# Optimization experiments

Hardware: AMD Instinct MI355X
Metric: run time of the kernel (lower is better)

Reference implementation:

```python
import jax, jax.numpy as jnp
import numpy as np
from jax import lax

N = 100000      # nodes
F_IN = 128      # dataset.num_features
H = 64          # hidden
E = 1600000     # edges
G = 1000        # graphs (equal-sized, contiguous)
PER = N // G    # nodes per graph = 100
K = 30          # sort-pool k
KS = 3          # conv1d kernel = num_layers


def setup_inputs() -> dict:
    key = jax.random.key(0)
    ks = jax.random.split(key, 20)
    lin = lambda k, i, o: (jax.random.normal(k, (i, o), jnp.float32) / np.sqrt(i)).astype(jnp.float32)
    return {
        "x": jax.random.normal(ks[0], (N, F_IN), jnp.float32),
        "src": jax.random.randint(ks[1], (E,), 0, N, dtype=jnp.int32),
        "dst": jax.random.randint(ks[2], (E,), 0, N, dtype=jnp.int32),
        "num_graphs": G,
        # SAGEConv 1: lin_l (aggr, with bias), lin_r (self, no bias)
        "wl1": lin(ks[3], F_IN, H), "wr1": lin(ks[4], F_IN, H), "b1": jnp.zeros((H,), jnp.float32),
        "wl2": lin(ks[5], H, H), "wr2": lin(ks[6], H, H), "b2": jnp.zeros((H,), jnp.float32),
        "wl3": lin(ks[7], H, H), "wr3": lin(ks[8], H, H), "b3": jnp.zeros((H,), jnp.float32),
        # Conv1d(hidden=64 -> 32, kernel=3): weight [O, I, K]
        "cw": (jax.random.normal(ks[9], (32, H, KS), jnp.float32) / np.sqrt(H * KS)).astype(jnp.float32),
        "cb": jnp.zeros((32,), jnp.float32),
        "w1": lin(ks[10], 32 * (K - KS + 1), H), "bb1": jnp.zeros((H,), jnp.float32),
        "w2": lin(ks[11], H, 1), "bb2": jnp.zeros((1,), jnp.float32),
    }


def _sage(x, src, dst, wl, wr, b, n):
    # PyG SAGEConv (mean aggr): lin_l(mean_{j->i} x_j) + lin_r(x_i)
    msum = jax.ops.segment_sum(x[src], dst, num_segments=n)           # [N, F]
    cnt = jax.ops.segment_sum(jnp.ones((src.shape[0],), x.dtype), dst, num_segments=n)
    mean = msum / jnp.maximum(cnt, 1.0)[:, None]
    return mean @ wl + b + x @ wr


def reference(x, src, dst, num_graphs, wl1, wr1, b1, wl2, wr2, b2, wl3, wr3, b3, cw, cb, w1, bb1, w2, bb2):
    n = x.shape[0]
    h = jax.nn.relu(_sage(x, src, dst, wl1, wr1, b1, n))
    h = jax.nn.relu(_sage(h, src, dst, wl2, wr2, b2, n))
    h = jax.nn.relu(_sage(h, src, dst, wl3, wr3, b3, n))
    # SortAggregation(k): per-graph, sort nodes by last feature channel (desc), keep top-k.
    # batch = contiguous equal-sized graphs -> dense reshape is exact.
    hg = h.reshape(num_graphs, PER, H)                                # [G, PER, H]
    order = jnp.argsort(-hg[:, :, -1], axis=1)[:, :K]                 # [G, K]
    topk = jnp.take_along_axis(hg, order[:, :, None], axis=1)         # [G, K, H]
    xc = jnp.transpose(topk, (0, 2, 1))                               # [G, H, K]
    y = lax.conv_general_dilated(xc, cw, (1,), 'VALID',
                                 dimension_numbers=('NCH', 'OIH', 'NCH'))
    y = jax.nn.relu(y + cb[None, :, None])                            # [G, 32, K-KS+1]
    y = y.reshape(num_graphs, -1)
    y = jax.nn.relu(y @ w1 + bb1)
    # dropout: eval mode -> identity
    return y @ w2 + bb2                                               # [G, 1]
```

## Files before the change

kernel.cpp:

```cpp
#include <hip/hip_runtime.h>

#define NN 100000
#define EE 1600000
#define GG 1000
#define PERG 100
#define KK 30
#define HH 64

#define NB 782
#define CAP 4096
#define CHB 4096

__global__ __launch_bounds__(1024) void zero_int(int* p, int n) {
  int i = blockIdx.x * 1024 + threadIdx.x;
  if (i < n) p[i] = 0;
}

__global__ __launch_bounds__(256) void bucket_kernel(const int* __restrict__ src,
                                                     const int* __restrict__ dst,
                                                     int* __restrict__ gcur,
                                                     int* __restrict__ pairs) {
  __shared__ int lhist[NB];
  __shared__ int lbase[NB];
  __shared__ int lcur[NB];
  const int t = threadIdx.x;
  const int c0 = blockIdx.x * CHB;
  const int c1 = min(c0 + CHB, EE);
  for (int b = t; b < NB; b += 256) {
    lhist[b] = 0;
    lcur[b] = 0;
  }
  __syncthreads();
  for (int e = c0 + t; e < c1; e += 256) atomicAdd(&lhist[dst[e] >> 7], 1);
  __syncthreads();
  for (int b = t; b < NB; b += 256) {
    int c = lhist[b];
    lbase[b] = c ? atomicAdd(&gcur[b], c) : 0;
  }
  __syncthreads();
  for (int e = c0 + t; e < c1; e += 256) {
    int d = dst[e];
    int b = d >> 7;
    int p = atomicAdd(&lcur[b], 1);
    pairs[b * CAP + lbase[b] + p] = (src[e] << 7) | (d & 127);
  }
}

__global__ __launch_bounds__(1024) void bucket_scan(const int* __restrict__ gcur,
                                                    int* __restrict__ bbase) {
  __shared__ int tmp[1024];
  const int t = threadIdx.x;
  int v = (t < NB) ? gcur[t] : 0;
  tmp[t] = v;
  __syncthreads();
  for (int off = 1; off < 1024; off <<= 1) {
    int u = (t >= off) ? tmp[t - off] : 0;
    __syncthreads();
    tmp[t] += u;
    __syncthreads();
  }
  if (t < NB) bbase[t] = tmp[t] - v;
}

__global__ __launch_bounds__(256) void csr_kernel(const int* __restrict__ gcur,
                                                  const int* __restrict__ bbase,
                                                  const int* __restrict__ pairs,
                                                  int* __restrict__ row_start,
                                                  int* __restrict__ cnt,
                                                  int* __restrict__ eidx) {
  __shared__ int vals[CAP];
  __shared__ int hist[128];
  __shared__ int offs[128];
  __shared__ int cur[128];
  const int b = blockIdx.x;
  const int t = threadIdx.x;
  const int nb = gcur[b];
  const int base = bbase[b];
  if (t < 128) {
    hist[t] = 0;
    cur[t] = 0;
  }
  __syncthreads();
  for (int i = t; i < nb; i += 256) {
    int v = pairs[b * CAP + i];
    vals[i] = v;
    atomicAdd(&hist[v & 127], 1);
  }
  __syncthreads();
  if (t < 128) {
    int s = 0;
    for (int m = 0; m < t; ++m) s += hist[m];
    offs[t] = s;
    int node = b * 128 + t;
    if (node < NN) {
      row_start[node] = base + s;
      cnt[node] = hist[t];
    }
  }
  __syncthreads();
  for (int i = t; i < nb; i += 256) {
    int v = vals[i];
    int ld = v & 127;
    int p = atomicAdd(&cur[ld], 1);
    eidx[base + offs[ld] + p] = v >> 7;
  }
}

template <int K>
__global__ __launch_bounds__(256) void proj_kernel(const float* __restrict__ X,
                                                   const float* __restrict__ WL,
                                                   const float* __restrict__ WR,
                                                   float* __restrict__ P,
                                                   float* __restrict__ R) {
  constexpr int BM = 128, BK = 32, XSP = 40, WSP = 144;
  __shared__ float xs[BM * XSP];
  __shared__ float ws[BK * WSP];
  const int t = threadIdx.x;
  const int row0 = blockIdx.x * BM;
  const int tc = t & 15, tr = t >> 4;
  const int wcol = tc * 8 + (tc >> 2) * 4;

  float acc[8][8];
#pragma unroll
  for (int i = 0; i < 8; ++i)
#pragma unroll
    for (int j = 0; j < 8; ++j) acc[i][j] = 0.f;

  for (int k0 = 0; k0 < K; k0 += BK) {
    __syncthreads();
    for (int idx = t; idx < BM * 8; idx += 256) {
      int r = idx >> 3, c = idx & 7;
      int row = row0 + r;
      float4 v = make_float4(0.f, 0.f, 0.f, 0.f);
      if (row < NN) v = *reinterpret_cast<const float4*>(&X[(size_t)row * K + k0 + c * 4]);
      *reinterpret_cast<float4*>(&xs[r * XSP + c * 4]) = v;
    }
    for (int idx = t; idx < BK * 16; idx += 256) {
      int kr = idx >> 4, c4 = idx & 15;
      int gcl = c4 >> 1;
      int off = gcl * 8 + (gcl >> 2) * 4 + (c4 & 1) * 4;
      *reinterpret_cast<float4*>(&ws[kr * WSP + off]) =
          *reinterpret_cast<const float4*>(&WL[(k0 + kr) * 64 + c4 * 4]);
      int g2 = gcl + 8;
      int off2 = g2 * 8 + (g2 >> 2) * 4 + (c4 & 1) * 4;
      *reinterpret_cast<float4*>(&ws[kr * WSP + off2]) =
          *reinterpret_cast<const float4*>(&WR[(k0 + kr) * 64 + c4 * 4]);
    }
    __syncthreads();
    for (int kk4 = 0; kk4 < BK; kk4 += 4) {
      float4 a[8];
#pragma unroll
      for (int i = 0; i < 8; ++i)
        a[i] = *reinterpret_cast<const float4*>(&xs[(tr + 16 * i) * XSP + kk4]);
#pragma unroll
      for (int kk = 0; kk < 4; ++kk) {
        float4 b0 = *reinterpret_cast<const float4*>(&ws[(kk4 + kk) * WSP + wcol]);
        float4 b1 = *reinterpret_cast<const float4*>(&ws[(kk4 + kk) * WSP + wcol + 4]);
        float bv[8] = {b0.x, b0.y, b0.z, b0.w, b1.x, b1.y, b1.z, b1.w};
#pragma unroll
        for (int i = 0; i < 8; ++i) {
          float av = (kk == 0) ? a[i].x : (kk == 1) ? a[i].y : (kk == 2) ? a[i].z : a[i].w;
#pragma unroll
          for (int j = 0; j < 8; ++j) acc[i][j] = fmaf(av, bv[j], acc[i][j]);
        }
      }
    }
  }

  float* OUT = (tc < 8) ? P : R;
  int cb = (tc & 7) * 8;
#pragma unroll
  for (int i = 0; i < 8; ++i) {
    int row = row0 + tr + 16 * i;
    if (row < NN) {
      *reinterpret_cast<float4*>(&OUT[(size_t)row * 64 + cb]) =
          make_float4(acc[i][0], acc[i][1], acc[i][2], acc[i][3]);
      *reinterpret_cast<float4*>(&OUT[(size_t)row * 64 + cb + 4]) =
          make_float4(acc[i][4], acc[i][5], acc[i][6], acc[i][7]);
    }
  }
}

__global__ __launch_bounds__(256) void agg_kernel(const float* __restrict__ P,
                                                  const float* __restrict__ R,
                                                  const float* __restrict__ bias,
                                                  const int* __restrict__ row_start,
                                                  const int* __restrict__ cnt,
                                                  const int* __restrict__ eidx,
                                                  float* __restrict__ h,
                                                  float* __restrict__ keys) {
  int wid = (blockIdx.x * 256 + threadIdx.x) >> 6;
  int lane = threadIdx.x & 63;
  if (wid >= NN) return;
  const int q = lane >> 4;
  const int ql = lane & 15;
  const int base = row_start[wid];
  const int deg = cnt[wid];
  float4 a0 = make_float4(0.f, 0.f, 0.f, 0.f);
  float4 a1 = make_float4(0.f, 0.f, 0.f, 0.f);

  for (int e0 = 0; e0 < deg; e0 += 64) {
    const int m = min(64, deg - e0);
    int idx = (lane < m) ? eidx[base + e0 + lane] : 0;
    for (int j = 0; j < m; j += 16) {
      const int eA = j + q, eB = j + 4 + q, eC = j + 8 + q, eD = j + 12 + q;
      const int sA = __shfl(idx, min(eA, m - 1));
      const int sB = __shfl(idx, min(eB, m - 1));
      const int sC = __shfl(idx, min(eC, m - 1));
      const int sD = __shfl(idx, min(eD, m - 1));
      const float wA = (eA < m) ? 1.f : 0.f;
      const float wB = (eB < m) ? 1.f : 0.f;
      const float wC = (eC < m) ? 1.f : 0.f;
      const float wD = (eD < m) ? 1.f : 0.f;
      float4 vA = *reinterpret_cast<const float4*>(&P[(size_t)sA * 64 + ql * 4]);
      float4 vB = *reinterpret_cast<const float4*>(&P[(size_t)sB * 64 + ql * 4]);
      float4 vC = *reinterpret_cast<const float4*>(&P[(size_t)sC * 64 + ql * 4]);
      float4 vD = *reinterpret_cast<const float4*>(&P[(size_t)sD * 64 + ql * 4]);
      a0.x = fmaf(wA, vA.x, a0.x); a0.y = fmaf(wA, vA.y, a0.y);
      a0.z = fmaf(wA, vA.z, a0.z); a0.w = fmaf(wA, vA.w, a0.w);
      a1.x = fmaf(wB, vB.x, a1.x); a1.y = fmaf(wB, vB.y, a1.y);
      a1.z = fmaf(wB, vB.z, a1.z); a1.w = fmaf(wB, vB.w, a1.w);
      a0.x = fmaf(wC, vC.x, a0.x); a0.y = fmaf(wC, vC.y, a0.y);
      a0.z = fmaf(wC, vC.z, a0.z); a0.w = fmaf(wC, vC.w, a0.w);
      a1.x = fmaf(wD, vD.x, a1.x); a1.y = fmaf(wD, vD.y, a1.y);
      a1.z = fmaf(wD, vD.z, a1.z); a1.w = fmaf(wD, vD.w, a1.w);
    }
  }

  float4 acc = make_float4(a0.x + a1.x, a0.y + a1.y, a0.z + a1.z, a0.w + a1.w);
#pragma unroll
  for (int d = 16; d < 64; d <<= 1) {
    acc.x += __shfl_xor(acc.x, d);
    acc.y += __shfl_xor(acc.y, d);
    acc.z += __shfl_xor(acc.z, d);
    acc.w += __shfl_xor(acc.w, d);
  }

  if (q == 0) {
    const float dv = fmaxf((float)deg, 1.0f);
    float4 r4 = *reinterpret_cast<const float4*>(&R[(size_t)wid * 64 + ql * 4]);
    float4 b4 = *reinterpret_cast<const float4*>(&bias[ql * 4]);
    float4 o;
    o.x = fmaxf(acc.x / dv + b4.x + r4.x, 0.f);
    o.y = fmaxf(acc.y / dv + b4.y + r4.y, 0.f);
    o.z = fmaxf(acc.z / dv + b4.z + r4.z, 0.f);
    o.w = fmaxf(acc.w / dv + b4.w + r4.w, 0.f);
    *reinterpret_cast<float4*>(&h[(size_t)wid * 64 + ql * 4]) = o;
    if (keys != nullptr && ql == 15) keys[wid] = o.w;
  }
}

__global__ __launch_bounds__(256) void head_kernel(const float* __restrict__ h,
                                                   const float* __restrict__ keysArr,
                                                   const float* __restrict__ cw,
                                                   const float* __restrict__ cb,
                                                   const float* __restrict__ w1,
                                                   const float* __restrict__ bb1,
                                                   const float* __restrict__ w2,
                                                   const float* __restrict__ bb2,
                                                   float* __restrict__ out) {
  __shared__ float key[PERG];
  __shared__ int sel[KK];
  __shared__ float feat[34 * 65];
  __shared__ float cwT[192 * 33];
  __shared__ float z[896];
  __shared__ float psum[256];
  const int g = blockIdx.x;
  const int t = threadIdx.x;

  for (int idx = t; idx < 32 * 192; idx += 256) {
    int o = idx / 192, k = idx % 192;
    cwT[k * 33 + o] = cw[idx];
  }
  if (t < PERG) key[t] = keysArr[g * PERG + t];
  __syncthreads();

  if (t < PERG) {
    float kv = key[t];
    int r = 0;
    for (int m = 0; m < PERG; ++m) {
      float km = key[m];
      r += (int)((km > kv) || (km == kv && m < t));
    }
    if (r < KK) sel[r] = t;
  }
  __syncthreads();

  for (int idx = t; idx < KK * HH; idx += 256) {
    int r = idx >> 6, f = idx & 63;
    feat[r * 65 + f] = h[(size_t)(g * PERG + sel[r]) * HH + f];
  }
  __syncthreads();

  {
    const int o = t & 31;
    const int pg = t >> 5;
    float zacc[4] = {0.f, 0.f, 0.f, 0.f};
    int i = 0, tt = 0;
    for (int k = 0; k < 192; ++k) {
      float c = cwT[k * 33 + o];
#pragma unroll
      for (int j = 0; j < 4; ++j) {
        int p = pg + 8 * j;
        zacc[j] = fmaf(c, feat[(p + tt) * 65 + i], zacc[j]);
      }
      if (++tt == 3) {
        tt = 0;
        ++i;
      }
    }
    float cbo = cb[o];
#pragma unroll
    for (int j = 0; j < 4; ++j) {
      int p = pg + 8 * j;
      if (p < 28) z[o * 28 + p] = fmaxf(zacc[j] + cbo, 0.f);
    }
  }
  __syncthreads();

  {
    const int hh = t & 63;
    const int quarter = t >> 6;
    const int q0 = quarter * 224;
    float acc = 0.f;
    for (int q = 0; q < 224; ++q)
      acc = fmaf(z[q0 + q], w1[(size_t)(q0 + q) * 64 + hh], acc);
    psum[t] = acc;
  }
  __syncthreads();

  if (t < 64) {
    float o1 = fmaxf(bb1[t] + psum[t] + psum[t + 64] + psum[t + 128] + psum[t + 192], 0.f);
    float v = o1 * w2[t];
#pragma unroll
    for (int off = 32; off > 0; off >>= 1) v += __shfl_down(v, off);
    if (t == 0) out[g] = v + bb2[0];
  }
}

extern "C" void kernel_launch(void* const* d_in, const int* in_sizes, int n_in,
                              void* d_out, int out_size, void* d_ws, size_t ws_size,
                              hipStream_t stream) {
  const float* x = (const float*)d_in[0];
  const int* src = (const int*)d_in[1];
  const int* dst = (const int*)d_in[2];
  const float* wl1 = (const float*)d_in[4];
  const float* wr1 = (const float*)d_in[5];
  const float* b1 = (const float*)d_in[6];
  const float* wl2 = (const float*)d_in[7];
  const float* wr2 = (const float*)d_in[8];
  const float* b2 = (const float*)d_in[9];
  const float* wl3 = (const float*)d_in[10];
  const float* wr3 = (const float*)d_in[11];
  const float* b3 = (const float*)d_in[12];
  const float* cw = (const float*)d_in[13];
  const float* cb = (const float*)d_in[14];
  const float* w1 = (const float*)d_in[15];
  const float* bb1 = (const float*)d_in[16];
  const float* w2 = (const float*)d_in[17];
  const float* bb2 = (const float*)d_in[18];
  float* out = (float*)d_out;

  char* w = (char*)d_ws;
  auto carve = [&](size_t bytes) {
    char* p = w;
    w += (bytes + 255) & ~(size_t)255;
    return p;
  };
  int* row_start = (int*)carve((size_t)NN * 4);
  int* cnt = (int*)carve((size_t)NN * 4);
  int* eidx = (int*)carve((size_t)EE * 4);
  float* P = (float*)carve((size_t)NN * 64 * 4);
  float* R = (float*)carve((size_t)NN * 64 * 4);
  float* hbuf = (float*)carve((size_t)NN * 64 * 4);
  float* keys = (float*)carve((size_t)NN * 4);
  int* gcur = (int*)carve((size_t)NB * 4);
  int* bbase = (int*)carve((size_t)NB * 4);
  int* pairs = (int*)P;

  zero_int<<<1, 1024, 0, stream>>>(gcur, NB);
  bucket_kernel<<<(EE + CHB - 1) / CHB, 256, 0, stream>>>(src, dst, gcur, pairs);
  bucket_scan<<<1, 1024, 0, stream>>>(gcur, bbase);
  csr_kernel<<<NB, 256, 0, stream>>>(gcur, bbase, pairs, row_start, cnt, eidx);

  const int projGrid = (NN + 127) / 128;
  const int aggGrid = (NN + 3) / 4;
  proj_kernel<128><<<projGrid, 256, 0, stream>>>(x, wl1, wr1, P, R);
  agg_kernel<<<aggGrid, 256, 0, stream>>>(P, R, b1, row_start, cnt, eidx, hbuf, nullptr);
  proj_kernel<64><<<projGrid, 256, 0, stream>>>(hbuf, wl2, wr2, P, R);
  agg_kernel<<<aggGrid, 256, 0, stream>>>(P, R, b2, row_start, cnt, eidx, hbuf, nullptr);
  proj_kernel<64><<<projGrid, 256, 0, stream>>>(hbuf, wl3, wr3, P, R);
  agg_kernel<<<aggGrid, 256, 0, stream>>>(P, R, b3, row_start, cnt, eidx, hbuf, keys);
  head_kernel<<<GG, 256, 0, stream>>>(hbuf, keys, cw, cb, w1, bb1, w2, bb2, out);
}
```

Baseline: 491.1 us.

## Fuse edge bucketing with first projection and fold bucket scan into CSR

The edge bucketing pass and the first-layer projection GEMM now run as one launch, with blocks split by index so the two independent jobs share the GPU. The bucket-offset scan kernel is removed: each CSR block computes its own base by reducing the preceding bucket counts. The pairs scratch moves from P to hbuf so it does not collide with the projection outputs. This saves two launches and lets the scatter and GEMM overlap, at the cost of redundant prefix reads in every CSR block and a larger shared allocation for the bucket blocks.

```diff
diff --git a/kernel.cpp b/kernel.cpp
--- a/kernel.cpp
+++ b/kernel.cpp
@@ -10,21 +10,24 @@
 #define NB 782
 #define CAP 4096
 #define CHB 4096
+#define BUCKET_BLOCKS ((EE + CHB - 1) / CHB)
+#define PROJ_BLOCKS ((NN + 127) / 128)
 
 __global__ __launch_bounds__(1024) void zero_int(int* p, int n) {
   int i = blockIdx.x * 1024 + threadIdx.x;
   if (i < n) p[i] = 0;
 }
 
-__global__ __launch_bounds__(256) void bucket_kernel(const int* __restrict__ src,
-                                                     const int* __restrict__ dst,
-                                                     int* __restrict__ gcur,
-                                                     int* __restrict__ pairs) {
-  __shared__ int lhist[NB];
-  __shared__ int lbase[NB];
-  __shared__ int lcur[NB];
+__device__ __forceinline__ void bucket_body(int bid, float* smem,
+                                            const int* __restrict__ src,
+                                            const int* __restrict__ dst,
+                                            int* __restrict__ gcur,
+                                            int* __restrict__ pairs) {
+  int* lhist = (int*)smem;
+  int* lbase = lhist + NB;
+  int* lcur = lbase + NB;
   const int t = threadIdx.x;
-  const int c0 = blockIdx.x * CHB;
+  const int c0 = bid * CHB;
   const int c1 = min(c0 + CHB, EE);
   for (int b = t; b < NB; b += 256) {
     lhist[b] = 0;
@@ -46,77 +49,18 @@
   }
 }
 
-__global__ __launch_bounds__(1024) void bucket_scan(const int* __restrict__ gcur,
-                                                    int* __restrict__ bbase) {
-  __shared__ int tmp[1024];
+template <int K>
+__device__ __forceinline__ void proj_body(int bid, float* smem,
+                                          const float* __restrict__ X,
+                                          const float* __restrict__ WL,
+                                          const float* __restrict__ WR,
+                                          float* __restrict__ P,
+                                          float* __restrict__ R) {
+  constexpr int BM = 128, BK = 32, XSP = 40, WSP = 144;
+  float* xs = smem;
+  float* ws = smem + BM * XSP;
   const int t = threadIdx.x;
-  int v = (t < NB) ? gcur[t] : 0;
-  tmp[t] = v;
-  __syncthreads();
-  for (int off = 1; off < 1024; off <<= 1) {
-    int u = (t >= off) ? tmp[t - off] : 0;
-    __syncthreads();
-    tmp[t] += u;
-    __syncthreads();
-  }
-  if (t < NB) bbase[t] = tmp[t] - v;
-}
-
-__global__ __launch_bounds__(256) void csr_kernel(const int* __restrict__ gcur,
-                                                  const int* __restrict__ bbase,
-                                                  const int* __restrict__ pairs,
-                                                  int* __restrict__ row_start,
-                                                  int* __restrict__ cnt,
-                                                  int* __restrict__ eidx) {
-  __shared__ int vals[CAP];
-  __shared__ int hist[128];
-  __shared__ int offs[128];
-  __shared__ int cur[128];
-  const int b = blockIdx.x;
-  const int t = threadIdx.x;
-  const int nb = gcur[b];
-  const int base = bbase[b];
-  if (t < 128) {
-    hist[t] = 0;
-    cur[t] = 0;
-  }
-  __syncthreads();
-  for (int i = t; i < nb; i += 256) {
-    int v = pairs[b * CAP + i];
-    vals[i] = v;
-    atomicAdd(&hist[v & 127], 1);
-  }
-  __syncthreads();
-  if (t < 128) {
-    int s = 0;
-    for (int m = 0; m < t; ++m) s += hist[m];
-    offs[t] = s;
-    int node = b * 128 + t;
-    if (node < NN) {
-      row_start[node] = base + s;
-      cnt[node] = hist[t];
-    }
-  }
-  __syncthreads();
-  for (int i = t; i < nb; i += 256) {
-    int v = vals[i];
-    int ld = v & 127;
-    int p = atomicAdd(&cur[ld], 1);
-    eidx[base + offs[ld] + p] = v >> 7;
-  }
-}
-
-template <int K>
-__global__ __launch_bounds__(256) void proj_kernel(const float* __restrict__ X,
-                                                   const float* __restrict__ WL,
-                                                   const float* __restrict__ WR,
-                                                   float* __restrict__ P,
-                                                   float* __restrict__ R) {
-  constexpr int BM = 128, BK = 32, XSP = 40, WSP = 144;
-  __shared__ float xs[BM * XSP];
-  __shared__ float ws[BK * WSP];
-  const int t = threadIdx.x;
-  const int row0 = blockIdx.x * BM;
+  const int row0 = bid * BM;
   const int tc = t & 15, tr = t >> 4;
   const int wcol = tc * 8 + (tc >> 2) * 4;
 
@@ -178,6 +122,81 @@
       *reinterpret_cast<float4*>(&OUT[(size_t)row * 64 + cb + 4]) =
           make_float4(acc[i][4], acc[i][5], acc[i][6], acc[i][7]);
     }
+  }
+}
+
+__global__ __launch_bounds__(256) void fused_bucket_proj(const int* __restrict__ src,
+                                                         const int* __restrict__ dst,
+                                                         int* __restrict__ gcur,
+                                                         int* __restrict__ pairs,
+                                                         const float* __restrict__ X,
+                                                         const float* __restrict__ WL,
+                                                         const float* __restrict__ WR,
+                                                         float* __restrict__ P,
+                                                         float* __restrict__ R) {
+  __shared__ float smem[128 * 40 + 32 * 144];
+  if (blockIdx.x < BUCKET_BLOCKS)
+    bucket_body(blockIdx.x, smem, src, dst, gcur, pairs);
+  else
+    proj_body<128>(blockIdx.x - BUCKET_BLOCKS, smem, X, WL, WR, P, R);
+}
+
+template <int K>
+__global__ __launch_bounds__(256) void proj_kernel(const float* __restrict__ X,
+                                                   const float* __restrict__ WL,
+                                                   const float* __restrict__ WR,
+                                                   float* __restrict__ P,
+                                                   float* __restrict__ R) {
+  __shared__ float smem[128 * 40 + 32 * 144];
+  proj_body<K>(blockIdx.x, smem, X, WL, WR, P, R);
+}
+
+__global__ __launch_bounds__(256) void csr_kernel(const int* __restrict__ gcur,
+                                                  const int* __restrict__ pairs,
+                                                  int* __restrict__ row_start,
+                                                  int* __restrict__ cnt,
+                                                  int* __restrict__ eidx) {
+  __shared__ int vals[CAP];
+  __shared__ int hist[128];
+  __shared__ int offs[128];
+  __shared__ int cur[128];
+  __shared__ int red[4];
+  const int b = blockIdx.x;
+  const int t = threadIdx.x;
+  int s = 0;
+  for (int i = t; i < b; i += 256) s += gcur[i];
+#pragma unroll
+  for (int off = 32; off > 0; off >>= 1) s += __shfl_xor(s, off);
+  if ((t & 63) == 0) red[t >> 6] = s;
+  if (t < 128) {
+    hist[t] = 0;
+    cur[t] = 0;
+  }
+  __syncthreads();
+  const int base = red[0] + red[1] + red[2] + red[3];
+  const int nb = gcur[b];
+  for (int i = t; i < nb; i += 256) {
+    int v = pairs[b * CAP + i];
+    vals[i] = v;
+    atomicAdd(&hist[v & 127], 1);
+  }
+  __syncthreads();
+  if (t < 128) {
+    int ss = 0;
+    for (int m = 0; m < t; ++m) ss += hist[m];
+    offs[t] = ss;
+    int node = b * 128 + t;
+    if (node < NN) {
+      row_start[node] = base + ss;
+      cnt[node] = hist[t];
+    }
+  }
+  __syncthreads();
+  for (int i = t; i < nb; i += 256) {
+    int v = vals[i];
+    int ld = v & 127;
+    int p = atomicAdd(&cur[ld], 1);
+    eidx[base + offs[ld] + p] = v >> 7;
   }
 }
 
@@ -375,21 +394,18 @@
   float* hbuf = (float*)carve((size_t)NN * 64 * 4);
   float* keys = (float*)carve((size_t)NN * 4);
   int* gcur = (int*)carve((size_t)NB * 4);
-  int* bbase = (int*)carve((size_t)NB * 4);
-  int* pairs = (int*)P;
+  int* pairs = (int*)hbuf;
 
   zero_int<<<1, 1024, 0, stream>>>(gcur, NB);
-  bucket_kernel<<<(EE + CHB - 1) / CHB, 256, 0, stream>>>(src, dst, gcur, pairs);
-  bucket_scan<<<1, 1024, 0, stream>>>(gcur, bbase);
-  csr_kernel<<<NB, 256, 0, stream>>>(gcur, bbase, pairs, row_start, cnt, eidx);
-
-  const int projGrid = (NN + 127) / 128;
+  fused_bucket_proj<<<BUCKET_BLOCKS + PROJ_BLOCKS, 256, 0, stream>>>(
+      src, dst, gcur, pairs, x, wl1, wr1, P, R);
+  csr_kernel<<<NB, 256, 0, stream>>>(gcur, pairs, row_start, cnt, eidx);
+
   const int aggGrid = (NN + 3) / 4;
-  proj_kernel<128><<<projGrid, 256, 0, stream>>>(x, wl1, wr1, P, R);
   agg_kernel<<<aggGrid, 256, 0, stream>>>(P, R, b1, row_start, cnt, eidx, hbuf, nullptr);
-  proj_kernel<64><<<projGrid, 256, 0, stream>>>(hbuf, wl2, wr2, P, R);
+  proj_kernel<64><<<PROJ_BLOCKS, 256, 0, stream>>>(hbuf, wl2, wr2, P, R);
   agg_kernel<<<aggGrid, 256, 0, stream>>>(P, R, b2, row_start, cnt, eidx, hbuf, nullptr);
-  proj_kernel<64><<<projGrid, 256, 0, stream>>>(hbuf, wl3, wr3, P, R);
+  proj_kernel<64><<<PROJ_BLOCKS, 256, 0, stream>>>(hbuf, wl3, wr3, P, R);
   agg_kernel<<<aggGrid, 256, 0, stream>>>(P, R, b3, row_start, cnt, eidx, hbuf, keys);
   head_kernel<<<GG, 256, 0, stream>>>(hbuf, keys, cw, cb, w1, bb1, w2, bb2, out);
 }
```

Measured after the change: 482.1 us. Within noise of the previous version (-1.8%).
